# Performance work log

Hardware: AMD Instinct MI355X
Metric: run time of the kernel (lower is better)

Reference implementation:

```python
import jax, jax.numpy as jnp
import numpy as np

# Minimal Mamba (alxndrTL mamba.py style) as used by MambaLithium.
# d_model=512, d_inner=1024 (expand=2), d_state=16, d_conv=4, dt_rank=32, n_layers=4.

EPS = 1e-5

def rmsnorm(x, w):
    # x: (B,L,D), w: (D,)
    return x * jax.lax.rsqrt(jnp.mean(x * x, axis=-1, keepdims=True) + EPS) * w

def causal_depthwise_conv(x, w, b):
    # x: (B,L,ED), w: (ED,K), b: (ED,)
    ED, K = w.shape
    xc = jnp.swapaxes(x, 1, 2)                       # (B,ED,L)
    k = w[:, None, :]                                # (ED,1,K) OIH
    y = jax.lax.conv_general_dilated(
        xc, k, window_strides=(1,), padding=[(K - 1, 0)],
        dimension_numbers=('NCH', 'OIH', 'NCH'), feature_group_count=ED)
    return jnp.swapaxes(y + b[None, :, None], 1, 2)  # (B,L,ED)

def selective_scan(xb, delta, Bm, Cm, A, D):
    # xb, delta: (B,L,ED); Bm, Cm: (B,L,N); A: (ED,N); D: (ED,)
    def step(h, inp):
        xt, dt, bt, ct = inp                          # (B,ED),(B,ED),(B,N),(B,N)
        dA = jnp.exp(dt[:, :, None] * A)              # (B,ED,N)
        dBx = (dt * xt)[:, :, None] * bt[:, None, :]  # (B,ED,N)
        h = dA * h + dBx
        y = jnp.einsum('ben,bn->be', h, ct)
        return h, y
    B_, _, ED = xb.shape
    N = A.shape[1]
    h0 = jnp.zeros((B_, ED, N), xb.dtype)
    xs = (jnp.swapaxes(xb, 0, 1), jnp.swapaxes(delta, 0, 1),
          jnp.swapaxes(Bm, 0, 1), jnp.swapaxes(Cm, 0, 1))
    _, ys = jax.lax.scan(step, h0, xs)                # ys: (L,B,ED)
    return jnp.swapaxes(ys, 0, 1) + xb * D

def mamba_block(x, in_w, conv_w, conv_b, xproj_w, dt_w, dt_b, A_log, Dp, out_w, dt_rank, d_state):
    # x: (B,L,D)
    xz = x @ in_w.T                                   # (B,L,2*ED)
    xb, z = jnp.split(xz, 2, axis=-1)
    xb = jax.nn.silu(causal_depthwise_conv(xb, conv_w, conv_b))
    dbc = xb @ xproj_w.T                              # (B,L,R+2N)
    dt, Bm, Cm = jnp.split(dbc, [dt_rank, dt_rank + d_state], axis=-1)
    delta = jax.nn.softplus(dt @ dt_w.T + dt_b)       # (B,L,ED)
    A = -jnp.exp(A_log)                               # (ED,N)
    y = selective_scan(xb, delta, Bm, Cm, A, Dp)
    y = y * jax.nn.silu(z)
    return y @ out_w.T                                # (B,L,D)

def reference(x, fc1_w, fc1_b, fc2_w, fc2_b, norm_w, in_proj_w, conv_w, conv_b,
              xproj_w, dtproj_w, dtproj_b, A_log, D_param, out_proj_w):
    n_layers = norm_w.shape[0]
    dt_rank = dtproj_w.shape[2]
    d_state = A_log.shape[2]
    h = x @ fc1_w.T + fc1_b                           # (B,L,D)
    for i in range(n_layers):
        h = h + mamba_block(rmsnorm(h, norm_w[i]), in_proj_w[i], conv_w[i], conv_b[i],
                            xproj_w[i], dtproj_w[i], dtproj_b[i], A_log[i], D_param[i],
                            out_proj_w[i], dt_rank, d_state)
    out = jax.nn.sigmoid(h @ fc2_w.T + fc2_b)         # (B,L,out_dim)
    return out.reshape(-1)

def setup_inputs() -> dict:
    key = jax.random.key(0)
    ks = jax.random.split(key, 12)
    B, L, Din, D, Dout, NL = 4, 1024, 32, 512, 1, 4
    ED, N, K, R = 1024, 16, 4, 32
    def rn(k, shape, scale):
        return jax.random.normal(k, shape, jnp.float32) * scale
    return {
        'x': jax.random.normal(ks[0], (B, L, Din), jnp.float32),
        'fc1_w': rn(ks[1], (D, Din), 0.1),
        'fc1_b': jnp.zeros((D,), jnp.float32),
        'fc2_w': rn(ks[2], (Dout, D), 0.1),
        'fc2_b': jnp.zeros((Dout,), jnp.float32),
        'norm_w': jnp.ones((NL, D), jnp.float32),
        'in_proj_w': rn(ks[3], (NL, 2 * ED, D), 0.02),
        'conv_w': rn(ks[4], (NL, ED, K), 0.2),
        'conv_b': jnp.zeros((NL, ED), jnp.float32),
        'xproj_w': rn(ks[5], (NL, R + 2 * N, ED), 0.02),
        'dtproj_w': rn(ks[6], (NL, ED, R), 0.1),
        'dtproj_b': rn(ks[7], (NL, ED), 0.1),
        'A_log': jnp.tile(jnp.log(jnp.arange(1, N + 1, dtype=jnp.float32))[None, None, :], (NL, ED, 1)),
        'D_param': jnp.ones((NL, ED), jnp.float32),
        'out_proj_w': rn(ks[8], (NL, D, ED), 0.02),
    }
```

## Files before the change

### kernel.cpp

```cpp
#include <hip/hip_runtime.h>
#include <hip/hip_bf16.h>
#include <cmath>

#define BB 4
#define LSEQ 1024
#define DIN 32
#define DM 512
#define EDIM 1024
#define NST 16
#define RANK 32
#define MTOK (BB*LSEQ)
#define NC 32
#define CH (LSEQ/NC)
#define MB 1048576ull

typedef __attribute__((ext_vector_type(8))) short bx8;
typedef __attribute__((ext_vector_type(4))) float fx4;
typedef __hip_bfloat16 bf;

__device__ __forceinline__ float sigmoidf_(float x){ return 1.f/(1.f+__expf(-x)); }
__device__ __forceinline__ float softplusf_(float x){ return fmaxf(x,0.f) + log1pf(__expf(-fabsf(x))); }
__device__ __forceinline__ float siluf_(float x){ return x * sigmoidf_(x); }

__device__ __forceinline__ void gl16(const bf* g, bf* l) {
  __builtin_amdgcn_global_load_lds(
      (const __attribute__((address_space(1))) void*)g,
      (__attribute__((address_space(3))) void*)l, 16, 0, 0);
}

template<int BM, int BN, int EPI>
__global__ __launch_bounds__(256) void gemm_k(const float* __restrict__ A,
    const float* __restrict__ W, const float* __restrict__ bias,
    float* __restrict__ C, int M, int N, int K, int lda, int ldw, int ldc)
{
  constexpr int BK = 16;
  constexpr int TX = BN/4;
  constexpr int TY = 256/TX;
  constexpr int TM = BM/TY;
  __shared__ float As[BK][BM];
  __shared__ float Ws[BK][BN];
  const int t = threadIdx.x;
  const int n0 = blockIdx.x*BN, m0 = blockIdx.y*BM;
  const int tx = t % TX, ty = t / TX;
  float acc[TM][4];
  #pragma unroll
  for (int i=0;i<TM;i++){ acc[i][0]=0.f;acc[i][1]=0.f;acc[i][2]=0.f;acc[i][3]=0.f; }

  for (int k0=0;k0<K;k0+=BK) {
    __syncthreads();
    for (int f=t; f<BM*4; f+=256) {
      int row=f>>2, kq=f&3;
      float4 v = *(const float4*)(A + (size_t)(m0+row)*lda + (k0+kq*4));
      As[kq*4+0][row]=v.x; As[kq*4+1][row]=v.y; As[kq*4+2][row]=v.z; As[kq*4+3][row]=v.w;
    }
    for (int f=t; f<BN*4; f+=256) {
      int row=f>>2, kq=f&3;
      float4 v = *(const float4*)(W + (size_t)(n0+row)*ldw + (k0+kq*4));
      Ws[kq*4+0][row]=v.x; Ws[kq*4+1][row]=v.y; Ws[kq*4+2][row]=v.z; Ws[kq*4+3][row]=v.w;
    }
    __syncthreads();
    #pragma unroll
    for (int kk=0;kk<BK;kk++) {
      float a[TM], b[4];
      #pragma unroll
      for (int j=0;j<4;j++) b[j] = Ws[kk][tx*4+j];
      #pragma unroll
      for (int i=0;i<TM;i++) a[i] = As[kk][ty*TM+i];
      #pragma unroll
      for (int i=0;i<TM;i++)
        #pragma unroll
        for (int j=0;j<4;j++) acc[i][j] = fmaf(a[i], b[j], acc[i][j]);
    }
  }
  #pragma unroll
  for (int i=0;i<TM;i++) {
    float* cp = C + (size_t)(m0+ty*TM+i)*ldc + n0 + tx*4;
    float4 r; r.x=acc[i][0]; r.y=acc[i][1]; r.z=acc[i][2]; r.w=acc[i][3];
    if constexpr (EPI==2) { const float* bp = bias + n0 + tx*4;
      r.x+=bp[0]; r.y+=bp[1]; r.z+=bp[2]; r.w+=bp[3]; }
    if constexpr (EPI==3) { const float* bp = bias + n0 + tx*4;
      r.x=softplusf_(r.x+bp[0]); r.y=softplusf_(r.y+bp[1]);
      r.z=softplusf_(r.z+bp[2]); r.w=softplusf_(r.w+bp[3]); }
    *(float4*)cp = r;
  }
}

template<int BM, int BN, int WR, int WC, int EPI>
__global__ __launch_bounds__(256) void gemm_mfma2_k(
    const bf* __restrict__ Ahi, const bf* __restrict__ Alo,
    const bf* __restrict__ Whi, const bf* __restrict__ Wlo,
    float* __restrict__ Cx, float* __restrict__ Cz, int nsplit,
    int M, int N, int K, int ldc)
{
  constexpr int WM = BM/WR, WN = BN/WC;
  constexpr int FM = WM/16, FN = WN/16;
  __shared__ bf sAh[BM*32], sAl[BM*32], sWh[BN*32], sWl[BN*32];
  const int t = threadIdx.x;
  const int w = t>>6, lane = t&63;
  const int wr = w%WR, wc = w/WR;
  const int lr = lane&15, lk = lane>>4;
  const int rowl = lane>>2, coll = (lane&3)*8;

  const int gx = gridDim.x;
  const int flat = blockIdx.y*gx + blockIdx.x;
  const int cpx = (gx*gridDim.y)>>3;
  const int logical = (flat&7)*cpx + (flat>>3);
  const int m0 = (logical/gx)*BM, n0 = (logical%gx)*BN;

  fx4 acc[FM][FN];
  #pragma unroll
  for (int i=0;i<FM;i++)
    #pragma unroll
    for (int j=0;j<FN;j++) acc[i][j] = fx4{0.f,0.f,0.f,0.f};

  for (int k0=0;k0<K;k0+=32) {
    __syncthreads();
    {
      const int rb = w*(BM/4);
      #pragma unroll
      for (int q=0;q<BM/64;q++) {
        int r = rb + q*16 + rowl;
        size_t g = (size_t)(m0+r)*K + k0 + coll;
        gl16(Ahi+g, &sAh[(rb+q*16)*32]);
        gl16(Alo+g, &sAl[(rb+q*16)*32]);
      }
    }
    {
      const int rb = w*(BN/4);
      #pragma unroll
      for (int q=0;q<BN/64;q++) {
        int r = rb + q*16 + rowl;
        size_t g = (size_t)(n0+r)*K + k0 + coll;
        gl16(Whi+g, &sWh[(rb+q*16)*32]);
        gl16(Wlo+g, &sWl[(rb+q*16)*32]);
      }
    }
    __syncthreads();
    bx8 ah[FM], al[FM], bh[FN], bl[FN];
    #pragma unroll
    for (int i=0;i<FM;i++) {
      int row = wr*WM + i*16 + lr;
      ah[i] = *(const bx8*)&sAh[row*32 + lk*8];
      al[i] = *(const bx8*)&sAl[row*32 + lk*8];
    }
    #pragma unroll
    for (int j=0;j<FN;j++) {
      int row = wc*WN + j*16 + lr;
      bh[j] = *(const bx8*)&sWh[row*32 + lk*8];
      bl[j] = *(const bx8*)&sWl[row*32 + lk*8];
    }
    #pragma unroll
    for (int i=0;i<FM;i++)
      #pragma unroll
      for (int j=0;j<FN;j++) {
        acc[i][j] = __builtin_amdgcn_mfma_f32_16x16x32_bf16(ah[i], bh[j], acc[i][j], 0,0,0);
        acc[i][j] = __builtin_amdgcn_mfma_f32_16x16x32_bf16(ah[i], bl[j], acc[i][j], 0,0,0);
        acc[i][j] = __builtin_amdgcn_mfma_f32_16x16x32_bf16(al[i], bh[j], acc[i][j], 0,0,0);
      }
  }
  #pragma unroll
  for (int j=0;j<FN;j++) {
    int coln = n0 + wc*WN + j*16 + lr;
    float* Cb; int cc;
    if (coln < nsplit) { Cb = Cx; cc = coln; } else { Cb = Cz; cc = coln - nsplit; }
    #pragma unroll
    for (int i=0;i<FM;i++) {
      #pragma unroll
      for (int r=0;r<4;r++) {
        int row = m0 + wr*WM + i*16 + lk*4 + r;
        if constexpr (EPI==1) Cb[(size_t)row*ldc+cc] += acc[i][j][r];
        else                  Cb[(size_t)row*ldc+cc]  = acc[i][j][r];
      }
    }
  }
}

__global__ __launch_bounds__(256) void split_k(const float* __restrict__ in,
    bf* __restrict__ hi, bf* __restrict__ lo, int n4)
{
  int i = blockIdx.x*256 + threadIdx.x;
  if (i >= n4) return;
  float4 v = ((const float4*)in)[i];
  float f[4] = {v.x, v.y, v.z, v.w};
  bf hh[4], ll[4];
  #pragma unroll
  for (int j=0;j<4;j++) {
    hh[j] = __float2bfloat16(f[j]);
    ll[j] = __float2bfloat16(f[j] - __bfloat162float(hh[j]));
  }
  *(float2*)(hi + 4*(size_t)i) = *(float2*)hh;
  *(float2*)(lo + 4*(size_t)i) = *(float2*)ll;
}

__global__ __launch_bounds__(256) void rmsnorm_k(const float* __restrict__ h,
    const float* __restrict__ nw, bf* __restrict__ hn_hi, bf* __restrict__ hn_lo)
{
  int m = blockIdx.x, t = threadIdx.x;
  const float* row = h + (size_t)m*DM;
  float v0 = row[t], v1 = row[t+256];
  float s = v0*v0 + v1*v1;
  #pragma unroll
  for (int off=32; off>=1; off>>=1) s += __shfl_xor(s, off, 64);
  __shared__ float red[4];
  if ((t&63)==0) red[t>>6] = s;
  __syncthreads();
  float tot = red[0]+red[1]+red[2]+red[3];
  float r = rsqrtf(tot*(1.0f/512.0f) + 1e-5f);
  float o0 = v0*r*nw[t], o1 = v1*r*nw[t+256];
  bf h0 = __float2bfloat16(o0), h1 = __float2bfloat16(o1);
  hn_hi[(size_t)m*DM+t]     = h0;
  hn_lo[(size_t)m*DM+t]     = __float2bfloat16(o0 - __bfloat162float(h0));
  hn_hi[(size_t)m*DM+t+256] = h1;
  hn_lo[(size_t)m*DM+t+256] = __float2bfloat16(o1 - __bfloat162float(h1));
}

__global__ __launch_bounds__(256) void conv_silu_k(const float* __restrict__ Xb,
    const float* __restrict__ cw, const float* __restrict__ cb, float* __restrict__ xbc)
{
  int idx = blockIdx.x*256 + threadIdx.x;
  int e = idx & (EDIM-1);
  int m = idx >> 10;
  int l = m & (LSEQ-1);
  float4 w = *(const float4*)(cw + e*4);
  const float* xp = Xb + (size_t)m*EDIM + e;
  float acc = cb[e] + w.w * xp[0];
  if (l>0) acc += w.z * xp[-EDIM];
  if (l>1) acc += w.y * xp[-2*EDIM];
  if (l>2) acc += w.x * xp[-3*EDIM];
  xbc[idx] = siluf_(acc);
}

__global__ __launch_bounds__(256) void wtrans_k(const float* __restrict__ W, float* __restrict__ Wt)
{
  __shared__ float tile[64][65];
  int kb = blockIdx.x;
  for (int i=threadIdx.x; i<4096; i+=256) {
    int n = i>>6, c = i&63;
    tile[n][c] = W[(size_t)n*EDIM + kb*64 + c];
  }
  __syncthreads();
  for (int i=threadIdx.x; i<4096; i+=256) {
    int kk = i>>6, n = i&63;
    Wt[((size_t)kb*64+kk)*64 + n] = tile[n][kk];
  }
}

__global__ __launch_bounds__(256) void xproj_part_k(const float* __restrict__ A,
    const float* __restrict__ Wt, float* __restrict__ Cp)
{
  constexpr int KC = 256;
  __shared__ float As[16][KC];
  const int mb = blockIdx.x;
  const int kc = blockIdx.y;
  const int t  = threadIdx.x;
  const float* ap = A + ((size_t)mb*16)*EDIM + kc*KC;
  #pragma unroll
  for (int q=0;q<4;q++) {
    int i = q*256 + t;
    int r = i>>6, c4 = i&63;
    float4 v = *(const float4*)(ap + (size_t)r*EDIM + c4*4);
    *(float4*)&As[r][c4*4] = v;
  }
  __syncthreads();
  const int m = t>>4, n0 = (t&15)*4;
  const float* wp = Wt + (size_t)kc*KC*64 + n0;
  float4 acc = {0.f,0.f,0.f,0.f};
  #pragma unroll 8
  for (int k=0;k<KC;k++) {
    float a = As[m][k];
    float4 w = *(const float4*)(wp + (size_t)k*64);
    acc.x = fmaf(a,w.x,acc.x); acc.y = fmaf(a,w.y,acc.y);
    acc.z = fmaf(a,w.z,acc.z); acc.w = fmaf(a,w.w,acc.w);
  }
  *(float4*)(Cp + ((size_t)kc*MTOK + (size_t)mb*16 + m)*64 + n0) = acc;
}

__global__ __launch_bounds__(256) void xproj_red_k(const float* __restrict__ Cp,
    float* __restrict__ C)
{
  int i = blockIdx.x*256 + threadIdx.x;
  const size_t stride = (size_t)MTOK*64/4;
  float4 a = ((const float4*)Cp)[i];
  float4 b = ((const float4*)Cp)[i + stride];
  float4 c = ((const float4*)Cp)[i + 2*stride];
  float4 d = ((const float4*)Cp)[i + 3*stride];
  float4 r; r.x=a.x+b.x+c.x+d.x; r.y=a.y+b.y+c.y+d.y;
  r.z=a.z+b.z+c.z+d.z; r.w=a.w+b.w+c.w+d.w;
  ((float4*)C)[i] = r;
}

__global__ __launch_bounds__(256,2) void scan_chunkA_k(const float* __restrict__ xbc,
    const float* __restrict__ dl, const float* __restrict__ dbc,
    const float* __restrict__ A_log,
    float* __restrict__ P, float* __restrict__ S)
{
  int ed = blockIdx.x*256 + threadIdx.x;
  int b = blockIdx.y, c = blockIdx.z;
  const int l0 = c*CH;
  __shared__ float Bs[CH][NST];
  for (int i=threadIdx.x; i<CH*NST; i+=256) {
    int row = i>>4, col = i&15;
    Bs[row][col] = dbc[((size_t)b*LSEQ + l0 + row)*64 + 32 + col];
  }
  __syncthreads();
  const float* dp = dl  + ((size_t)b*LSEQ + l0)*EDIM + ed;
  const float* xp = xbc + ((size_t)b*LSEQ + l0)*EDIM + ed;
  float dt[CH], xv[CH];
  #pragma unroll
  for (int l=0;l<CH;l++){ dt[l]=dp[(size_t)l*EDIM]; xv[l]=xp[(size_t)l*EDIM]; }
  float a[NST], hs[NST], pp[NST];
  #pragma unroll
  for (int n=0;n<NST;n++){ a[n] = -__expf(A_log[ed*NST+n]); hs[n]=0.f; pp[n]=1.f; }
  #pragma unroll
  for (int l=0;l<CH;l++) {
    float dx = dt[l]*xv[l];
    #pragma unroll
    for (int n=0;n<NST;n++) {
      float dA = __expf(dt[l]*a[n]);
      hs[n] = fmaf(dA, hs[n], dx*Bs[l][n]);
      pp[n] *= dA;
    }
  }
  size_t base = (((size_t)b*NC + c)*NST)*EDIM + ed;
  #pragma unroll
  for (int n=0;n<NST;n++) { P[base + (size_t)n*EDIM] = pp[n]; S[base + (size_t)n*EDIM] = hs[n]; }
}

__global__ __launch_bounds__(256) void scan_combine_k(float* __restrict__ PH, const float* __restrict__ S)
{
  int t = blockIdx.x*256 + threadIdx.x;
  int b = blockIdx.y;
  const size_t stride = (size_t)NST*EDIM;
  size_t b0 = (size_t)b*NC*stride + t;
  float p[NC], s[NC];
  #pragma unroll
  for (int c=0;c<NC;c++){ p[c]=PH[b0+(size_t)c*stride]; s[c]=S[b0+(size_t)c*stride]; }
  float H = 0.f;
  #pragma unroll
  for (int c=0;c<NC;c++){ PH[b0+(size_t)c*stride] = H; H = fmaf(p[c], H, s[c]); }
}

__global__ __launch_bounds__(256,2) void scan_chunkC_k(const float* __restrict__ xbc,
    const float* __restrict__ dl, const float* __restrict__ dbc,
    const float* __restrict__ A_log, const float* __restrict__ Dp,
    const float* __restrict__ Hinit, const float* __restrict__ Z,
    bf* __restrict__ yz_hi, bf* __restrict__ yz_lo)
{
  int ed = blockIdx.x*256 + threadIdx.x;
  int b = blockIdx.y, c = blockIdx.z;
  const int l0 = c*CH;
  __shared__ float BCs[CH][32];
  for (int i=threadIdx.x; i<CH*32; i+=256) {
    int row = i>>5, col = i&31;
    BCs[row][col] = dbc[((size_t)b*LSEQ + l0 + row)*64 + 32 + col];
  }
  __syncthreads();
  const float* dp = dl  + ((size_t)b*LSEQ + l0)*EDIM + ed;
  const float* xp = xbc + ((size_t)b*LSEQ + l0)*EDIM + ed;
  const float* zp = Z   + ((size_t)b*LSEQ + l0)*EDIM + ed;
  float dt[CH], xv[CH], zv[CH];
  #pragma unroll
  for (int l=0;l<CH;l++){ dt[l]=dp[(size_t)l*EDIM]; xv[l]=xp[(size_t)l*EDIM]; zv[l]=zp[(size_t)l*EDIM]; }
  float a[NST], hs[NST];
  size_t base = (((size_t)b*NC + c)*NST)*EDIM + ed;
  #pragma unroll
  for (int n=0;n<NST;n++){ a[n] = -__expf(A_log[ed*NST+n]); hs[n] = Hinit[base + (size_t)n*EDIM]; }
  float Dv = Dp[ed];
  bf* yh = yz_hi + ((size_t)b*LSEQ + l0)*EDIM + ed;
  bf* yl = yz_lo + ((size_t)b*LSEQ + l0)*EDIM + ed;
  #pragma unroll
  for (int l=0;l<CH;l++) {
    float dx = dt[l]*xv[l];
    float yv = xv[l]*Dv;
    #pragma unroll
    for (int n=0;n<NST;n++) {
      float dA = __expf(dt[l]*a[n]);
      hs[n] = fmaf(dA, hs[n], dx*BCs[l][n]);
      yv = fmaf(hs[n], BCs[l][16+n], yv);
    }
    float g = yv * siluf_(zv[l]);
    bf gh = __float2bfloat16(g);
    yh[(size_t)l*EDIM] = gh;
    yl[(size_t)l*EDIM] = __float2bfloat16(g - __bfloat162float(gh));
  }
}

__global__ __launch_bounds__(64) void fc2_k(const float* __restrict__ h,
    const float* __restrict__ w, const float* __restrict__ b, float* __restrict__ out)
{
  int m = blockIdx.x, t = threadIdx.x;
  float s = 0.f;
  #pragma unroll
  for (int j=0;j<8;j++) { int k = t + j*64; s = fmaf(h[(size_t)m*DM+k], w[k], s); }
  #pragma unroll
  for (int off=32; off>=1; off>>=1) s += __shfl_xor(s, off, 64);
  if (t==0) out[m] = sigmoidf_(s + b[0]);
}

extern "C" void kernel_launch(void* const* d_in, const int* in_sizes, int n_in,
                              void* d_out, int out_size, void* d_ws, size_t ws_size,
                              hipStream_t stream) {
  const float* x         = (const float*)d_in[0];
  const float* fc1_w     = (const float*)d_in[1];
  const float* fc1_b     = (const float*)d_in[2];
  const float* fc2_w     = (const float*)d_in[3];
  const float* fc2_b     = (const float*)d_in[4];
  const float* norm_w    = (const float*)d_in[5];
  const float* in_proj_w = (const float*)d_in[6];
  const float* conv_w    = (const float*)d_in[7];
  const float* conv_b    = (const float*)d_in[8];
  const float* xproj_w   = (const float*)d_in[9];
  const float* dtproj_w  = (const float*)d_in[10];
  const float* dtproj_b  = (const float*)d_in[11];
  const float* A_log     = (const float*)d_in[12];
  const float* D_param   = (const float*)d_in[13];
  const float* out_proj_w= (const float*)d_in[14];
  float* out = (float*)d_out;

  char* w8 = (char*)d_ws;
  float* h    = (float*)(w8 +  0*MB);
  float* Xb   = (float*)(w8 +  8*MB);
  float* PH   = (float*)(w8 +  8*MB);
  float* Z    = (float*)(w8 + 24*MB);
  float* xbc  = (float*)(w8 + 40*MB);
  float* dl   = (float*)(w8 + 56*MB);
  float* dbcw = (float*)(w8 + 72*MB);
  bf*    win_hi = (bf*)(w8 + 73*MB);
  float* Wt     = (float*)(w8 + 73*MB);
  bf*    win_lo = (bf*)(w8 + 75*MB);
  bf*    wout_hi= (bf*)(w8 + 77*MB);
  bf*    wout_lo= (bf*)(w8 + 78*MB);
  bf*    hn_hi  = (bf*)(w8 + 79*MB);
  bf*    hn_lo  = (bf*)(w8 + 83*MB);
  float* Send   = (float*)(w8 + 79*MB);
  float* Cp     = (float*)(w8 + 79*MB);
  bf*    yz_hi  = (bf*)(w8 + 87*MB);
  bf*    yz_lo  = (bf*)(w8 + 95*MB);

  gemm_k<128,64,2><<<dim3(DM/64, MTOK/128), 256, 0, stream>>>(
      x, fc1_w, fc1_b, h, MTOK, DM, DIN, DIN, DIN, DM);

  for (int i=0;i<4;i++) {
    rmsnorm_k<<<MTOK, 256, 0, stream>>>(h, norm_w + (size_t)i*DM, hn_hi, hn_lo);
    split_k<<<(2048*512/4)/256, 256, 0, stream>>>(
        in_proj_w + (size_t)i*2048*DM, win_hi, win_lo, 2048*512/4);
    gemm_mfma2_k<128,128,2,2,0><<<dim3(2048/128, MTOK/128), 256, 0, stream>>>(
        hn_hi, hn_lo, win_hi, win_lo, Xb, Z, 1024, MTOK, 2048, DM, EDIM);
    conv_silu_k<<<(MTOK*EDIM)/256, 256, 0, stream>>>(
        Xb, conv_w + (size_t)i*EDIM*4, conv_b + (size_t)i*EDIM, xbc);
    wtrans_k<<<16, 256, 0, stream>>>(xproj_w + (size_t)i*64*EDIM, Wt);
    xproj_part_k<<<dim3(MTOK/16, 4), 256, 0, stream>>>(xbc, Wt, Cp);
    xproj_red_k<<<(MTOK*64/4)/256, 256, 0, stream>>>(Cp, dbcw);
    gemm_k<128,64,3><<<dim3(EDIM/64, MTOK/128), 256, 0, stream>>>(
        dbcw, dtproj_w + (size_t)i*EDIM*RANK, dtproj_b + (size_t)i*EDIM, dl,
        MTOK, EDIM, RANK, 64, RANK, EDIM);
    scan_chunkA_k<<<dim3(EDIM/256, BB, NC), 256, 0, stream>>>(
        xbc, dl, dbcw, A_log + (size_t)i*EDIM*NST, PH, Send);
    scan_combine_k<<<dim3(NST*EDIM/256, BB), 256, 0, stream>>>(PH, Send);
    scan_chunkC_k<<<dim3(EDIM/256, BB, NC), 256, 0, stream>>>(
        xbc, dl, dbcw, A_log + (size_t)i*EDIM*NST, D_param + (size_t)i*EDIM, PH,
        Z, yz_hi, yz_lo);
    split_k<<<(512*1024/4)/256, 256, 0, stream>>>(
        out_proj_w + (size_t)i*DM*EDIM, wout_hi, wout_lo, 512*1024/4);
    gemm_mfma2_k<64,64,2,2,1><<<dim3(DM/64, MTOK/64), 256, 0, stream>>>(
        yz_hi, yz_lo, wout_hi, wout_lo, h, h, DM, MTOK, DM, EDIM, DM);
  }

  fc2_k<<<MTOK, 64, 0, stream>>>(h, fc2_w, fc2_b, out);
}
```

Baseline: 884.3 us.

## Double-buffer MFMA GEMM shared tiles and fuse prep kernels into one launch

The split-bf16 MFMA GEMM now ping-pongs two shared-memory buffers, issuing the next K-tile load before computing on the current one, with one barrier per iteration instead of two. RMSNorm, the in/out projection weight splits and the xproj weight transpose are merged into a single block-indexed prep kernel, removing three launches per layer. The Wt buffer moves to a separate workspace region so it no longer aliases the weight splits. The cost is doubled LDS use in the GEMM, which may lower occupancy.

After: 863.2 us. -2.4%, faster.

```diff
diff --git a/kernel.cpp b/kernel.cpp
--- a/kernel.cpp
+++ b/kernel.cpp
@@ -94,7 +94,7 @@
 {
   constexpr int WM = BM/WR, WN = BN/WC;
   constexpr int FM = WM/16, FN = WN/16;
-  __shared__ bf sAh[BM*32], sAl[BM*32], sWh[BN*32], sWl[BN*32];
+  __shared__ bf sAh[2][BM*32], sAl[2][BM*32], sWh[2][BN*32], sWl[2][BN*32];
   const int t = threadIdx.x;
   const int w = t>>6, lane = t&63;
   const int wr = w%WR, wc = w/WR;
@@ -113,16 +113,15 @@
     #pragma unroll
     for (int j=0;j<FN;j++) acc[i][j] = fx4{0.f,0.f,0.f,0.f};
 
-  for (int k0=0;k0<K;k0+=32) {
-    __syncthreads();
+  auto stage = [&](int buf, int k0) {
     {
       const int rb = w*(BM/4);
       #pragma unroll
       for (int q=0;q<BM/64;q++) {
         int r = rb + q*16 + rowl;
         size_t g = (size_t)(m0+r)*K + k0 + coll;
-        gl16(Ahi+g, &sAh[(rb+q*16)*32]);
-        gl16(Alo+g, &sAl[(rb+q*16)*32]);
+        gl16(Ahi+g, &sAh[buf][(rb+q*16)*32]);
+        gl16(Alo+g, &sAl[buf][(rb+q*16)*32]);
       }
     }
     {
@@ -131,23 +130,30 @@
       for (int q=0;q<BN/64;q++) {
         int r = rb + q*16 + rowl;
         size_t g = (size_t)(n0+r)*K + k0 + coll;
-        gl16(Whi+g, &sWh[(rb+q*16)*32]);
-        gl16(Wlo+g, &sWl[(rb+q*16)*32]);
+        gl16(Whi+g, &sWh[buf][(rb+q*16)*32]);
+        gl16(Wlo+g, &sWl[buf][(rb+q*16)*32]);
       }
     }
-    __syncthreads();
+  };
+
+  const int NT = K/32;
+  stage(0, 0);
+  __syncthreads();
+  int cur = 0;
+  for (int tt=0; tt<NT; ++tt) {
+    if (tt+1 < NT) stage(cur^1, (tt+1)*32);
     bx8 ah[FM], al[FM], bh[FN], bl[FN];
     #pragma unroll
     for (int i=0;i<FM;i++) {
       int row = wr*WM + i*16 + lr;
-      ah[i] = *(const bx8*)&sAh[row*32 + lk*8];
-      al[i] = *(const bx8*)&sAl[row*32 + lk*8];
+      ah[i] = *(const bx8*)&sAh[cur][row*32 + lk*8];
+      al[i] = *(const bx8*)&sAl[cur][row*32 + lk*8];
     }
     #pragma unroll
     for (int j=0;j<FN;j++) {
       int row = wc*WN + j*16 + lr;
-      bh[j] = *(const bx8*)&sWh[row*32 + lk*8];
-      bl[j] = *(const bx8*)&sWl[row*32 + lk*8];
+      bh[j] = *(const bx8*)&sWh[cur][row*32 + lk*8];
+      bl[j] = *(const bx8*)&sWl[cur][row*32 + lk*8];
     }
     #pragma unroll
     for (int i=0;i<FM;i++)
@@ -157,6 +163,8 @@
         acc[i][j] = __builtin_amdgcn_mfma_f32_16x16x32_bf16(ah[i], bl[j], acc[i][j], 0,0,0);
         acc[i][j] = __builtin_amdgcn_mfma_f32_16x16x32_bf16(al[i], bh[j], acc[i][j], 0,0,0);
       }
+    __syncthreads();
+    cur ^= 1;
   }
   #pragma unroll
   for (int j=0;j<FN;j++) {
@@ -175,11 +183,9 @@
   }
 }
 
-__global__ __launch_bounds__(256) void split_k(const float* __restrict__ in,
-    bf* __restrict__ hi, bf* __restrict__ lo, int n4)
-{
-  int i = blockIdx.x*256 + threadIdx.x;
-  if (i >= n4) return;
+__device__ __forceinline__ void split4_(const float* __restrict__ in,
+    bf* __restrict__ hi, bf* __restrict__ lo, int i)
+{
   float4 v = ((const float4*)in)[i];
   float f[4] = {v.x, v.y, v.z, v.w};
   bf hh[4], ll[4];
@@ -192,26 +198,48 @@
   *(float2*)(lo + 4*(size_t)i) = *(float2*)ll;
 }
 
-__global__ __launch_bounds__(256) void rmsnorm_k(const float* __restrict__ h,
-    const float* __restrict__ nw, bf* __restrict__ hn_hi, bf* __restrict__ hn_lo)
-{
-  int m = blockIdx.x, t = threadIdx.x;
-  const float* row = h + (size_t)m*DM;
-  float v0 = row[t], v1 = row[t+256];
-  float s = v0*v0 + v1*v1;
-  #pragma unroll
-  for (int off=32; off>=1; off>>=1) s += __shfl_xor(s, off, 64);
-  __shared__ float red[4];
-  if ((t&63)==0) red[t>>6] = s;
-  __syncthreads();
-  float tot = red[0]+red[1]+red[2]+red[3];
-  float r = rsqrtf(tot*(1.0f/512.0f) + 1e-5f);
-  float o0 = v0*r*nw[t], o1 = v1*r*nw[t+256];
-  bf h0 = __float2bfloat16(o0), h1 = __float2bfloat16(o1);
-  hn_hi[(size_t)m*DM+t]     = h0;
-  hn_lo[(size_t)m*DM+t]     = __float2bfloat16(o0 - __bfloat162float(h0));
-  hn_hi[(size_t)m*DM+t+256] = h1;
-  hn_lo[(size_t)m*DM+t+256] = __float2bfloat16(o1 - __bfloat162float(h1));
+__global__ __launch_bounds__(256) void prep_k(
+    const float* __restrict__ h, const float* __restrict__ nw,
+    bf* __restrict__ hn_hi, bf* __restrict__ hn_lo,
+    const float* __restrict__ in_w, bf* __restrict__ win_hi, bf* __restrict__ win_lo,
+    const float* __restrict__ out_w, bf* __restrict__ wout_hi, bf* __restrict__ wout_lo,
+    const float* __restrict__ xw, float* __restrict__ Wt)
+{
+  __shared__ float smem[64*65];
+  const int bid = blockIdx.x, t = threadIdx.x;
+  if (bid < 4096) {
+    const float* row = h + (size_t)bid*DM;
+    float v0 = row[t], v1 = row[t+256];
+    float s = v0*v0 + v1*v1;
+    #pragma unroll
+    for (int off=32; off>=1; off>>=1) s += __shfl_xor(s, off, 64);
+    if ((t&63)==0) smem[t>>6] = s;
+    __syncthreads();
+    float tot = smem[0]+smem[1]+smem[2]+smem[3];
+    float r = rsqrtf(tot*(1.0f/512.0f) + 1e-5f);
+    float o0 = v0*r*nw[t], o1 = v1*r*nw[t+256];
+    bf h0 = __float2bfloat16(o0), h1 = __float2bfloat16(o1);
+    hn_hi[(size_t)bid*DM+t]     = h0;
+    hn_lo[(size_t)bid*DM+t]     = __float2bfloat16(o0 - __bfloat162float(h0));
+    hn_hi[(size_t)bid*DM+t+256] = h1;
+    hn_lo[(size_t)bid*DM+t+256] = __float2bfloat16(o1 - __bfloat162float(h1));
+  } else if (bid < 5120) {
+    split4_(in_w, win_hi, win_lo, (bid-4096)*256 + t);
+  } else if (bid < 5632) {
+    split4_(out_w, wout_hi, wout_lo, (bid-5120)*256 + t);
+  } else {
+    float (*tile)[65] = (float(*)[65])smem;
+    const int kb = bid - 5632;
+    for (int i=t; i<4096; i+=256) {
+      int n = i>>6, c = i&63;
+      tile[n][c] = xw[(size_t)n*EDIM + kb*64 + c];
+    }
+    __syncthreads();
+    for (int i=t; i<4096; i+=256) {
+      int kk = i>>6, n = i&63;
+      Wt[((size_t)kb*64+kk)*64 + n] = tile[n][kk];
+    }
+  }
 }
 
 __global__ __launch_bounds__(256) void conv_silu_k(const float* __restrict__ Xb,
@@ -228,21 +256,6 @@
   if (l>1) acc += w.y * xp[-2*EDIM];
   if (l>2) acc += w.x * xp[-3*EDIM];
   xbc[idx] = siluf_(acc);
-}
-
-__global__ __launch_bounds__(256) void wtrans_k(const float* __restrict__ W, float* __restrict__ Wt)
-{
-  __shared__ float tile[64][65];
-  int kb = blockIdx.x;
-  for (int i=threadIdx.x; i<4096; i+=256) {
-    int n = i>>6, c = i&63;
-    tile[n][c] = W[(size_t)n*EDIM + kb*64 + c];
-  }
-  __syncthreads();
-  for (int i=threadIdx.x; i<4096; i+=256) {
-    int kk = i>>6, n = i&63;
-    Wt[((size_t)kb*64+kk)*64 + n] = tile[n][kk];
-  }
 }
 
 __global__ __launch_bounds__(256) void xproj_part_k(const float* __restrict__ A,
@@ -426,7 +439,6 @@
   float* dl   = (float*)(w8 + 56*MB);
   float* dbcw = (float*)(w8 + 72*MB);
   bf*    win_hi = (bf*)(w8 + 73*MB);
-  float* Wt     = (float*)(w8 + 73*MB);
   bf*    win_lo = (bf*)(w8 + 75*MB);
   bf*    wout_hi= (bf*)(w8 + 77*MB);
   bf*    wout_lo= (bf*)(w8 + 78*MB);
@@ -436,19 +448,21 @@
   float* Cp     = (float*)(w8 + 79*MB);
   bf*    yz_hi  = (bf*)(w8 + 87*MB);
   bf*    yz_lo  = (bf*)(w8 + 95*MB);
+  float* Wt     = (float*)(w8 + 103*MB);
 
   gemm_k<128,64,2><<<dim3(DM/64, MTOK/128), 256, 0, stream>>>(
       x, fc1_w, fc1_b, h, MTOK, DM, DIN, DIN, DIN, DM);
 
   for (int i=0;i<4;i++) {
-    rmsnorm_k<<<MTOK, 256, 0, stream>>>(h, norm_w + (size_t)i*DM, hn_hi, hn_lo);
-    split_k<<<(2048*512/4)/256, 256, 0, stream>>>(
-        in_proj_w + (size_t)i*2048*DM, win_hi, win_lo, 2048*512/4);
+    prep_k<<<5648, 256, 0, stream>>>(
+        h, norm_w + (size_t)i*DM, hn_hi, hn_lo,
+        in_proj_w + (size_t)i*2048*DM, win_hi, win_lo,
+        out_proj_w + (size_t)i*DM*EDIM, wout_hi, wout_lo,
+        xproj_w + (size_t)i*64*EDIM, Wt);
     gemm_mfma2_k<128,128,2,2,0><<<dim3(2048/128, MTOK/128), 256, 0, stream>>>(
         hn_hi, hn_lo, win_hi, win_lo, Xb, Z, 1024, MTOK, 2048, DM, EDIM);
     conv_silu_k<<<(MTOK*EDIM)/256, 256, 0, stream>>>(
         Xb, conv_w + (size_t)i*EDIM*4, conv_b + (size_t)i*EDIM, xbc);
-    wtrans_k<<<16, 256, 0, stream>>>(xproj_w + (size_t)i*64*EDIM, Wt);
     xproj_part_k<<<dim3(MTOK/16, 4), 256, 0, stream>>>(xbc, Wt, Cp);
     xproj_red_k<<<(MTOK*64/4)/256, 256, 0, stream>>>(Cp, dbcw);
     gemm_k<128,64,3><<<dim3(EDIM/64, MTOK/128), 256, 0, stream>>>(
@@ -460,8 +474,6 @@
     scan_chunkC_k<<<dim3(EDIM/256, BB, NC), 256, 0, stream>>>(
         xbc, dl, dbcw, A_log + (size_t)i*EDIM*NST, D_param + (size_t)i*EDIM, PH,
         Z, yz_hi, yz_lo);
-    split_k<<<(512*1024/4)/256, 256, 0, stream>>>(
-        out_proj_w + (size_t)i*DM*EDIM, wout_hi, wout_lo, 512*1024/4);
     gemm_mfma2_k<64,64,2,2,1><<<dim3(DM/64, MTOK/64), 256, 0, stream>>>(
         yz_hi, yz_lo, wout_hi, wout_lo, h, h, DM, MTOK, DM, EDIM, DM);
   }
```
